# Kernel tuning notes

Hardware: AMD Instinct MI355X
Metric: run time of the kernel (lower is better)

Reference implementation:

```python
import jax, jax.numpy as jnp
import numpy as np

IN, U = 256, 512
UNFOLDS = 6

def setup_inputs() -> dict:
    key = jax.random.key(0)
    ks = jax.random.split(key, 16)
    B = 512
    inputs = jax.random.normal(ks[0], (B, IN), dtype=jnp.float32)
    state = jax.random.normal(ks[1], (B, U), dtype=jnp.float32)
    # parameters, initialized like the torch module
    sensory_mu = jax.random.uniform(ks[2], (IN, U), minval=0.3, maxval=0.8)
    sensory_sigma = jax.random.uniform(ks[3], (IN, U), minval=3.0, maxval=8.0)
    sensory_W = jax.random.uniform(ks[4], (IN, U), minval=0.01, maxval=1.0)
    sensory_erev = (2.0 * jax.random.randint(ks[5], (IN, U), 0, 2).astype(jnp.float32) - 1.0)
    mu = jax.random.uniform(ks[6], (U, U), minval=0.3, maxval=0.8)
    sigma = jax.random.uniform(ks[7], (U, U), minval=3.0, maxval=8.0)
    W = jax.random.uniform(ks[8], (U, U), minval=0.01, maxval=1.0)
    erev = (2.0 * jax.random.randint(ks[9], (U, U), 0, 2).astype(jnp.float32) - 1.0)
    vleak = jax.random.uniform(ks[10], (U,), minval=-0.2, maxval=0.2)
    gleak = jnp.ones((U,), dtype=jnp.float32)   # gleak_init_min == max == 1.0
    cm_t = jnp.full((U,), 0.5, dtype=jnp.float32)  # cm_init_min == max == 0.5
    input_w = jnp.ones((IN,), dtype=jnp.float32)
    input_b = jnp.zeros((IN,), dtype=jnp.float32)
    return dict(inputs=inputs, state=state, input_w=input_w, input_b=input_b,
                sensory_mu=sensory_mu, sensory_sigma=sensory_sigma,
                sensory_W=sensory_W, sensory_erev=sensory_erev,
                mu=mu, sigma=sigma, W=W, erev=erev,
                vleak=vleak, gleak=gleak, cm_t=cm_t)

def _syn_sigmoid(v, mu, sigma):
    # v: [B, N] -> [B, N, 1]; mu, sigma: [N, M]; result [B, N, M]
    return jax.nn.sigmoid(sigma * (v[..., None] - mu))

def reference(inputs, state, input_w, input_b, sensory_mu, sensory_sigma,
              sensory_W, sensory_erev, mu, sigma, W, erev, vleak, gleak, cm_t):
    # Affine input mapping
    x = inputs * input_w + input_b                       # [B, IN]
    # sensory synapses (computed once)
    sens_act = sensory_W * _syn_sigmoid(x, sensory_mu, sensory_sigma)  # [B, IN, U]
    w_num_s = jnp.sum(sens_act * sensory_erev, axis=1)   # [B, U]
    w_den_s = jnp.sum(sens_act, axis=1)                  # [B, U]
    # semi-implicit ODE unfold (6 fixed steps)
    v_pre = state
    for _ in range(UNFOLDS):
        w_act = W * _syn_sigmoid(v_pre, mu, sigma)       # [B, U, U]
        w_num = jnp.sum(w_act * erev, axis=1) + w_num_s  # [B, U]
        w_den = jnp.sum(w_act, axis=1) + w_den_s         # [B, U]
        numerator = cm_t * v_pre + gleak * vleak + w_num
        denominator = cm_t + gleak + w_den
        v_pre = numerator / denominator
    return v_pre  # module returns (next_state, next_state); both identical
```

## Files before the change

### kernel.cpp

```cpp
#include <hip/hip_runtime.h>

#define IN_DIM 256
#define U_DIM  512
#define L2E    1.44269504088896340736f

__global__ void k_fuse(const float* __restrict__ mu, const float* __restrict__ sigma,
                       const float* __restrict__ W, const float* __restrict__ erev,
                       const float* __restrict__ smu, const float* __restrict__ ssig,
                       const float* __restrict__ sW, const float* __restrict__ serev,
                       float2* __restrict__ sm2, float* __restrict__ wep,
                       float4* __restrict__ sf4) {
    int i = blockIdx.x * blockDim.x + threadIdx.x;
    const int UU = U_DIM * U_DIM;
    const int SU = IN_DIM * U_DIM;
    if (i < UU) {
        float s = sigma[i] * L2E;
        sm2[i] = make_float2(s, mu[i] * s);
        wep[i] = W[i] * erev[i];
    } else if (i < UU + SU) {
        int j = i - UU;
        float s = ssig[j] * L2E;
        float w = sW[j];
        sf4[j] = make_float4(s, smu[j] * s, w * serev[j], w);
    }
}

__global__ __launch_bounds__(512, 8) void k_sensory(
    const float* __restrict__ inputs, const float* __restrict__ input_w,
    const float* __restrict__ input_b, const float4* __restrict__ sf4,
    float* __restrict__ wnum_s, float* __restrict__ wden_s) {
    __shared__ __align__(16) float xs[4 * IN_DIM];
    __shared__ float red[8 * 4 * 64 * 2];
    const int tid = threadIdx.x;
    const int b0 = blockIdx.x * 4;
    const int u0 = blockIdx.y * 64;

    #pragma unroll
    for (int k = 0; k < 2; ++k) {
        int idx = tid + k * 512;
        int r = idx >> 8, i = idx & 255;
        xs[idx] = fmaf(inputs[(b0 + r) * IN_DIM + i], input_w[i], input_b[i]);
    }
    __syncthreads();

    const int ul = tid & 63;
    const int strip = tid >> 6;
    const int u = u0 + ul;
    float nacc[4], dacc[4];
    #pragma unroll
    for (int r = 0; r < 4; ++r) { nacc[r] = 0.f; dacc[r] = 0.f; }

    const int i0 = strip * 32;
    for (int ic = 0; ic < 32; ic += 4) {
        const int i = i0 + ic;
        float4 q0 = sf4[(i + 0) * U_DIM + u];
        float4 q1 = sf4[(i + 1) * U_DIM + u];
        float4 q2 = sf4[(i + 2) * U_DIM + u];
        float4 q3 = sf4[(i + 3) * U_DIM + u];
        #pragma unroll
        for (int r = 0; r < 4; ++r) {
            const float4 x4 = *reinterpret_cast<const float4*>(&xs[r * IN_DIM + i]);
            {
                float e = __builtin_amdgcn_exp2f(fmaf(-q0.x, x4.x, q0.y));
                float p = __builtin_amdgcn_rcpf(1.f + e);
                nacc[r] = fmaf(q0.z, p, nacc[r]); dacc[r] = fmaf(q0.w, p, dacc[r]);
            }
            {
                float e = __builtin_amdgcn_exp2f(fmaf(-q1.x, x4.y, q1.y));
                float p = __builtin_amdgcn_rcpf(1.f + e);
                nacc[r] = fmaf(q1.z, p, nacc[r]); dacc[r] = fmaf(q1.w, p, dacc[r]);
            }
            {
                float e = __builtin_amdgcn_exp2f(fmaf(-q2.x, x4.z, q2.y));
                float p = __builtin_amdgcn_rcpf(1.f + e);
                nacc[r] = fmaf(q2.z, p, nacc[r]); dacc[r] = fmaf(q2.w, p, dacc[r]);
            }
            {
                float e = __builtin_amdgcn_exp2f(fmaf(-q3.x, x4.w, q3.y));
                float p = __builtin_amdgcn_rcpf(1.f + e);
                nacc[r] = fmaf(q3.z, p, nacc[r]); dacc[r] = fmaf(q3.w, p, dacc[r]);
            }
        }
    }
    #pragma unroll
    for (int r = 0; r < 4; ++r) {
        red[(((strip * 4 + r) * 64) + ul) * 2 + 0] = nacc[r];
        red[(((strip * 4 + r) * 64) + ul) * 2 + 1] = dacc[r];
    }
    __syncthreads();
    if (tid < 4 * 64) {
        const int r = tid >> 6, uu = tid & 63;
        float n = 0.f, d = 0.f;
        #pragma unroll
        for (int s = 0; s < 8; ++s) {
            n += red[(((s * 4 + r) * 64) + uu) * 2 + 0];
            d += red[(((s * 4 + r) * 64) + uu) * 2 + 1];
        }
        wnum_s[(b0 + r) * U_DIM + (u0 + uu)] = n;
        wden_s[(b0 + r) * U_DIM + (u0 + uu)] = d;
    }
}

__global__ __launch_bounds__(512, 8) void k_unfold(
    const float* __restrict__ vin,
    const float2* __restrict__ sm2, const float* __restrict__ wep,
    const float* __restrict__ wnum_s, const float* __restrict__ wden_s,
    const float* __restrict__ vleak, const float* __restrict__ gleak,
    const float* __restrict__ cm, float* __restrict__ vout) {
    __shared__ __align__(16) float vs[8 * U_DIM];
    __shared__ float red_n[8 * 8 * 32];
    __shared__ float red_d[8 * 8 * 32];
    const int tid = threadIdx.x;
    const int b0 = blockIdx.x * 8;
    const int u0 = blockIdx.y * 32;

    #pragma unroll
    for (int k = 0; k < 2; ++k) {
        int idx = tid + k * 512;
        reinterpret_cast<float4*>(vs)[idx] =
            reinterpret_cast<const float4*>(vin + (size_t)b0 * U_DIM)[idx];
    }
    __syncthreads();

    const int lane = tid & 63;
    const int w = tid >> 6;
    const int ulh = lane & 31;
    const int ih = lane >> 5;
    const int strip = w * 2 + ih;
    const int u = u0 + ulh;
    const int i0 = strip * 32;

    float nacc[8], dacc[8];
    #pragma unroll
    for (int r = 0; r < 8; ++r) { nacc[r] = 0.f; dacc[r] = 0.f; }

    for (int ic = 0; ic < 32; ic += 4) {
        const int i = i0 + ic;
        float2 q0 = sm2[(i + 0) * U_DIM + u];
        float2 q1 = sm2[(i + 1) * U_DIM + u];
        float2 q2 = sm2[(i + 2) * U_DIM + u];
        float2 q3 = sm2[(i + 3) * U_DIM + u];
        float we0 = wep[(i + 0) * U_DIM + u];
        float we1 = wep[(i + 1) * U_DIM + u];
        float we2 = wep[(i + 2) * U_DIM + u];
        float we3 = wep[(i + 3) * U_DIM + u];
        float w0 = fabsf(we0), w1 = fabsf(we1), w2 = fabsf(we2), w3 = fabsf(we3);
        #pragma unroll
        for (int r = 0; r < 8; ++r) {
            const float4 v4 = *reinterpret_cast<const float4*>(&vs[r * U_DIM + i]);
            {
                float e = __builtin_amdgcn_exp2f(fmaf(-q0.x, v4.x, q0.y));
                float p = __builtin_amdgcn_rcpf(1.f + e);
                nacc[r] = fmaf(we0, p, nacc[r]); dacc[r] = fmaf(w0, p, dacc[r]);
            }
            {
                float e = __builtin_amdgcn_exp2f(fmaf(-q1.x, v4.y, q1.y));
                float p = __builtin_amdgcn_rcpf(1.f + e);
                nacc[r] = fmaf(we1, p, nacc[r]); dacc[r] = fmaf(w1, p, dacc[r]);
            }
            {
                float e = __builtin_amdgcn_exp2f(fmaf(-q2.x, v4.z, q2.y));
                float p = __builtin_amdgcn_rcpf(1.f + e);
                nacc[r] = fmaf(we2, p, nacc[r]); dacc[r] = fmaf(w2, p, dacc[r]);
            }
            {
                float e = __builtin_amdgcn_exp2f(fmaf(-q3.x, v4.w, q3.y));
                float p = __builtin_amdgcn_rcpf(1.f + e);
                nacc[r] = fmaf(we3, p, nacc[r]); dacc[r] = fmaf(w3, p, dacc[r]);
            }
        }
    }

    #pragma unroll
    for (int r = 0; r < 8; ++r) {
        nacc[r] += __shfl_xor(nacc[r], 32);
        dacc[r] += __shfl_xor(dacc[r], 32);
    }
    if (lane < 32) {
        #pragma unroll
        for (int r = 0; r < 8; ++r) {
            red_n[(w * 8 + r) * 32 + ulh] = nacc[r];
            red_d[(w * 8 + r) * 32 + ulh] = dacc[r];
        }
    }
    __syncthreads();
    if (tid < 8 * 32) {
        const int r = tid >> 5, uu = tid & 31;
        float n = 0.f, d = 0.f;
        #pragma unroll
        for (int s = 0; s < 8; ++s) {
            n += red_n[(s * 8 + r) * 32 + uu];
            d += red_d[(s * 8 + r) * 32 + uu];
        }
        const int gu = u0 + uu, gb = b0 + r;
        float vold = vs[r * U_DIM + gu];
        float gl = gleak[gu], c = cm[gu];
        float num = fmaf(c, vold, fmaf(gl, vleak[gu], n + wnum_s[gb * U_DIM + gu]));
        float den = c + gl + d + wden_s[gb * U_DIM + gu];
        vout[gb * U_DIM + gu] = num * __builtin_amdgcn_rcpf(den);
    }
}

__global__ __launch_bounds__(512) void k_mono(
    const float* __restrict__ inputs, const float* __restrict__ state,
    const float* __restrict__ input_w, const float* __restrict__ input_b,
    const float* __restrict__ smu, const float* __restrict__ ssig,
    const float* __restrict__ sW, const float* __restrict__ serev,
    const float* __restrict__ mu, const float* __restrict__ sigma,
    const float* __restrict__ W, const float* __restrict__ erev,
    const float* __restrict__ vleak, const float* __restrict__ gleak,
    const float* __restrict__ cm, float* __restrict__ out) {
    __shared__ float xs[IN_DIM];
    __shared__ float vsh[U_DIM];
    const int b = blockIdx.x, u = threadIdx.x;
    if (u < IN_DIM) xs[u] = fmaf(inputs[b * IN_DIM + u], input_w[u], input_b[u]);
    vsh[u] = state[b * U_DIM + u];
    __syncthreads();
    float ns = 0.f, ds = 0.f;
    for (int i = 0; i < IN_DIM; ++i) {
        int pi = i * U_DIM + u;
        float e = __builtin_amdgcn_exp2f((smu[pi] - xs[i]) * (ssig[pi] * L2E));
        float p = __builtin_amdgcn_rcpf(1.f + e);
        float a = sW[pi] * p;
        ns = fmaf(a, serev[pi], ns);
        ds += a;
    }
    const float c = cm[u], gl = gleak[u], glvl = gl * vleak[u];
    for (int t = 0; t < 6; ++t) {
        float n = ns, d = ds;
        for (int i = 0; i < U_DIM; ++i) {
            int pi = i * U_DIM + u;
            float e = __builtin_amdgcn_exp2f((mu[pi] - vsh[i]) * (sigma[pi] * L2E));
            float p = __builtin_amdgcn_rcpf(1.f + e);
            float a = W[pi] * p;
            n = fmaf(a, erev[pi], n);
            d += a;
        }
        float vn = (fmaf(c, vsh[u], glvl) + n) / (c + gl + d);
        __syncthreads();
        vsh[u] = vn;
        __syncthreads();
    }
    out[b * U_DIM + u] = vsh[u];
}

extern "C" void kernel_launch(void* const* d_in, const int* in_sizes, int n_in,
                              void* d_out, int out_size, void* d_ws, size_t ws_size,
                              hipStream_t stream) {
    const float* inputs  = (const float*)d_in[0];
    const float* state   = (const float*)d_in[1];
    const float* input_w = (const float*)d_in[2];
    const float* input_b = (const float*)d_in[3];
    const float* smu     = (const float*)d_in[4];
    const float* ssig    = (const float*)d_in[5];
    const float* sW      = (const float*)d_in[6];
    const float* serev   = (const float*)d_in[7];
    const float* mu      = (const float*)d_in[8];
    const float* sigma   = (const float*)d_in[9];
    const float* W       = (const float*)d_in[10];
    const float* erev    = (const float*)d_in[11];
    const float* vleak   = (const float*)d_in[12];
    const float* gleak   = (const float*)d_in[13];
    const float* cm      = (const float*)d_in[14];
    float* out = (float*)d_out;

    const int B = in_sizes[1] / U_DIM;
    const size_t BU = (size_t)B * U_DIM;
    const size_t UU = (size_t)U_DIM * U_DIM;
    const size_t SU = (size_t)IN_DIM * U_DIM;
    const size_t need = (3 * BU + 3 * UU + 4 * SU) * sizeof(float);

    if (ws_size >= need) {
        float* f      = (float*)d_ws;
        float* wnum_s = f;
        float* wden_s = f + BU;
        float* vbuf   = f + 2 * BU;
        float2* sm2   = (float2*)(f + 3 * BU);
        float* wep    = f + 3 * BU + 2 * UU;
        float4* sf4   = (float4*)(f + 3 * BU + 3 * UU);

        const int nfuse = (int)(UU + SU);
        k_fuse<<<(nfuse + 255) / 256, 256, 0, stream>>>(mu, sigma, W, erev,
                                                        smu, ssig, sW, serev,
                                                        sm2, wep, sf4);
        dim3 sgrid(B / 4, U_DIM / 64);
        k_sensory<<<sgrid, 512, 0, stream>>>(inputs, input_w, input_b, sf4, wnum_s, wden_s);
        dim3 ugrid(B / 8, U_DIM / 32);
        const float* vin = state;
        float* pong[2] = { vbuf, out };
        for (int t = 0; t < 6; ++t) {
            float* vo = pong[t & 1];
            k_unfold<<<ugrid, 512, 0, stream>>>(vin, sm2, wep, wnum_s, wden_s,
                                                vleak, gleak, cm, vo);
            vin = vo;
        }
    } else {
        k_mono<<<B, U_DIM, 0, stream>>>(inputs, state, input_w, input_b,
                                        smu, ssig, sW, serev, mu, sigma, W, erev,
                                        vleak, gleak, cm, out);
    }
}
```

Before: 210.3 us.

## Replace transcendental sigmoid with packed polynomial exp2 and shared reciprocal

```diff
diff --git a/kernel.cpp b/kernel.cpp
--- a/kernel.cpp
+++ b/kernel.cpp
@@ -3,6 +3,47 @@
 #define IN_DIM 256
 #define U_DIM  512
 #define L2E    1.44269504088896340736f
+
+typedef float f32x2 __attribute__((ext_vector_type(2)));
+typedef float f32x4 __attribute__((ext_vector_type(4)));
+
+__device__ __forceinline__ f32x2 vfma2(f32x2 a, f32x2 b, f32x2 c) {
+    return __builtin_elementwise_fma(a, b, c);
+}
+
+__device__ __forceinline__ float exp2scale(float y) {
+    unsigned s = (__float_as_uint(y) << 23) + 0x3F800000u;
+    return __uint_as_float(s);
+}
+
+__device__ __forceinline__ void quad_sig(f32x2 t01, f32x2 t23,
+                                         f32x2& p01, f32x2& p23) {
+    const float CM = 12582912.0f;
+    const float c4 = 0.00961813f, c3 = 0.05550411f,
+                c2 = 0.24022651f, c1 = 0.69314718f;
+    t01.x = fminf(fmaxf(t01.x, -100.f), 14.f);
+    t01.y = fminf(fmaxf(t01.y, -100.f), 14.f);
+    t23.x = fminf(fmaxf(t23.x, -100.f), 14.f);
+    t23.y = fminf(fmaxf(t23.y, -100.f), 14.f);
+    f32x2 y01 = t01 + (f32x2)(CM);
+    f32x2 y23 = t23 + (f32x2)(CM);
+    f32x2 f01 = t01 - (y01 - (f32x2)(CM));
+    f32x2 f23 = t23 - (y23 - (f32x2)(CM));
+    f32x2 q01 = vfma2((f32x2)(c4), f01, (f32x2)(c3));
+    f32x2 q23 = vfma2((f32x2)(c4), f23, (f32x2)(c3));
+    q01 = vfma2(q01, f01, (f32x2)(c2));  q23 = vfma2(q23, f23, (f32x2)(c2));
+    q01 = vfma2(q01, f01, (f32x2)(c1));  q23 = vfma2(q23, f23, (f32x2)(c1));
+    q01 = vfma2(q01, f01, (f32x2)(1.f)); q23 = vfma2(q23, f23, (f32x2)(1.f));
+    f32x2 sc01 = { exp2scale(y01.x), exp2scale(y01.y) };
+    f32x2 sc23 = { exp2scale(y23.x), exp2scale(y23.y) };
+    f32x2 d01 = vfma2(q01, sc01, (f32x2)(1.f));
+    f32x2 d23 = vfma2(q23, sc23, (f32x2)(1.f));
+    float a = d01.x * d01.y, b = d23.x * d23.y;
+    float R = __builtin_amdgcn_rcpf(a * b);
+    float Ra = R * a, Rb = R * b;
+    p01 = (f32x2){ Rb * d01.y, Rb * d01.x };
+    p23 = (f32x2){ Ra * d23.y, Ra * d23.x };
+}
 
 __global__ void k_fuse(const float* __restrict__ mu, const float* __restrict__ sigma,
                        const float* __restrict__ W, const float* __restrict__ erev,
@@ -25,89 +66,95 @@
     }
 }
 
-__global__ __launch_bounds__(512, 8) void k_sensory(
+__global__ __launch_bounds__(512, 4) void k_sensory(
     const float* __restrict__ inputs, const float* __restrict__ input_w,
     const float* __restrict__ input_b, const float4* __restrict__ sf4,
     float* __restrict__ wnum_s, float* __restrict__ wden_s) {
-    __shared__ __align__(16) float xs[4 * IN_DIM];
-    __shared__ float red[8 * 4 * 64 * 2];
+    __shared__ __align__(16) float xs2[IN_DIM * 8];
+    __shared__ float red_n[8 * 8 * 32];
+    __shared__ float red_d[8 * 8 * 32];
     const int tid = threadIdx.x;
-    const int b0 = blockIdx.x * 4;
-    const int u0 = blockIdx.y * 64;
+    const int b0 = blockIdx.x * 8;
+    const int u0 = blockIdx.y * 32;
 
     #pragma unroll
-    for (int k = 0; k < 2; ++k) {
+    for (int k = 0; k < 4; ++k) {
         int idx = tid + k * 512;
         int r = idx >> 8, i = idx & 255;
-        xs[idx] = fmaf(inputs[(b0 + r) * IN_DIM + i], input_w[i], input_b[i]);
-    }
-    __syncthreads();
-
-    const int ul = tid & 63;
-    const int strip = tid >> 6;
-    const int u = u0 + ul;
-    float nacc[4], dacc[4];
+        xs2[i * 8 + r] = fmaf(inputs[(b0 + r) * IN_DIM + i], input_w[i], input_b[i]);
+    }
+    __syncthreads();
+
+    const int lane = tid & 63;
+    const int w = tid >> 6;
+    const int ulh = lane & 31;
+    const int ih = lane >> 5;
+    const int strip = w * 2 + ih;
+    const int u = u0 + ulh;
+    const int i0 = strip * 16;
+
+    f32x2 na01 = {0,0}, na23 = {0,0}, na45 = {0,0}, na67 = {0,0};
+    f32x2 da01 = {0,0}, da23 = {0,0}, da45 = {0,0}, da67 = {0,0};
+
+    #pragma unroll 2
+    for (int ic = 0; ic < 16; ++ic) {
+        const int i = i0 + ic;
+        const float4 q = sf4[i * U_DIM + u];
+        const float sgn = -q.x, ms = q.y, we = q.z, wa = q.w;
+        f32x4 va = *reinterpret_cast<const f32x4*>(&xs2[i * 8]);
+        f32x4 vb = *reinterpret_cast<const f32x4*>(&xs2[i * 8 + 4]);
+        f32x2 p01, p23, p45, p67;
+        {
+            f32x2 t01 = vfma2((f32x2)(sgn), va.xy, (f32x2)(ms));
+            f32x2 t23 = vfma2((f32x2)(sgn), va.zw, (f32x2)(ms));
+            quad_sig(t01, t23, p01, p23);
+        }
+        {
+            f32x2 t45 = vfma2((f32x2)(sgn), vb.xy, (f32x2)(ms));
+            f32x2 t67 = vfma2((f32x2)(sgn), vb.zw, (f32x2)(ms));
+            quad_sig(t45, t67, p45, p67);
+        }
+        na01 = vfma2((f32x2)(we), p01, na01); da01 = vfma2((f32x2)(wa), p01, da01);
+        na23 = vfma2((f32x2)(we), p23, na23); da23 = vfma2((f32x2)(wa), p23, da23);
+        na45 = vfma2((f32x2)(we), p45, na45); da45 = vfma2((f32x2)(wa), p45, da45);
+        na67 = vfma2((f32x2)(we), p67, na67); da67 = vfma2((f32x2)(wa), p67, da67);
+    }
+
+    float nacc[8] = { na01.x, na01.y, na23.x, na23.y, na45.x, na45.y, na67.x, na67.y };
+    float dacc[8] = { da01.x, da01.y, da23.x, da23.y, da45.x, da45.y, da67.x, da67.y };
     #pragma unroll
-    for (int r = 0; r < 4; ++r) { nacc[r] = 0.f; dacc[r] = 0.f; }
-
-    const int i0 = strip * 32;
-    for (int ic = 0; ic < 32; ic += 4) {
-        const int i = i0 + ic;
-        float4 q0 = sf4[(i + 0) * U_DIM + u];
-        float4 q1 = sf4[(i + 1) * U_DIM + u];
-        float4 q2 = sf4[(i + 2) * U_DIM + u];
-        float4 q3 = sf4[(i + 3) * U_DIM + u];
+    for (int r = 0; r < 8; ++r) {
+        nacc[r] += __shfl_xor(nacc[r], 32);
+        dacc[r] += __shfl_xor(dacc[r], 32);
+    }
+    if (lane < 32) {
         #pragma unroll
-        for (int r = 0; r < 4; ++r) {
-            const float4 x4 = *reinterpret_cast<const float4*>(&xs[r * IN_DIM + i]);
-            {
-                float e = __builtin_amdgcn_exp2f(fmaf(-q0.x, x4.x, q0.y));
-                float p = __builtin_amdgcn_rcpf(1.f + e);
-                nacc[r] = fmaf(q0.z, p, nacc[r]); dacc[r] = fmaf(q0.w, p, dacc[r]);
-            }
-            {
-                float e = __builtin_amdgcn_exp2f(fmaf(-q1.x, x4.y, q1.y));
-                float p = __builtin_amdgcn_rcpf(1.f + e);
-                nacc[r] = fmaf(q1.z, p, nacc[r]); dacc[r] = fmaf(q1.w, p, dacc[r]);
-            }
-            {
-                float e = __builtin_amdgcn_exp2f(fmaf(-q2.x, x4.z, q2.y));
-                float p = __builtin_amdgcn_rcpf(1.f + e);
-                nacc[r] = fmaf(q2.z, p, nacc[r]); dacc[r] = fmaf(q2.w, p, dacc[r]);
-            }
-            {
-                float e = __builtin_amdgcn_exp2f(fmaf(-q3.x, x4.w, q3.y));
-                float p = __builtin_amdgcn_rcpf(1.f + e);
-                nacc[r] = fmaf(q3.z, p, nacc[r]); dacc[r] = fmaf(q3.w, p, dacc[r]);
-            }
-        }
-    }
-    #pragma unroll
-    for (int r = 0; r < 4; ++r) {
-        red[(((strip * 4 + r) * 64) + ul) * 2 + 0] = nacc[r];
-        red[(((strip * 4 + r) * 64) + ul) * 2 + 1] = dacc[r];
-    }
-    __syncthreads();
-    if (tid < 4 * 64) {
-        const int r = tid >> 6, uu = tid & 63;
+        for (int r = 0; r < 8; ++r) {
+            red_n[(w * 8 + r) * 32 + ulh] = nacc[r];
+            red_d[(w * 8 + r) * 32 + ulh] = dacc[r];
+        }
+    }
+    __syncthreads();
+    if (tid < 8 * 32) {
+        const int r = tid >> 5, uu = tid & 31;
         float n = 0.f, d = 0.f;
         #pragma unroll
         for (int s = 0; s < 8; ++s) {
-            n += red[(((s * 4 + r) * 64) + uu) * 2 + 0];
-            d += red[(((s * 4 + r) * 64) + uu) * 2 + 1];
+            n += red_n[(s * 8 + r) * 32 + uu];
+            d += red_d[(s * 8 + r) * 32 + uu];
         }
         wnum_s[(b0 + r) * U_DIM + (u0 + uu)] = n;
         wden_s[(b0 + r) * U_DIM + (u0 + uu)] = d;
     }
 }
 
-__global__ __launch_bounds__(512, 8) void k_unfold(
+__global__ __launch_bounds__(512, 4) void k_unfold(
     const float* __restrict__ vin,
     const float2* __restrict__ sm2, const float* __restrict__ wep,
     const float* __restrict__ wnum_s, const float* __restrict__ wden_s,
     const float* __restrict__ vleak, const float* __restrict__ gleak,
     const float* __restrict__ cm, float* __restrict__ vout) {
-    __shared__ __align__(16) float vs[8 * U_DIM];
+    __shared__ __align__(16) float vs2[U_DIM * 8];
     __shared__ float red_n[8 * 8 * 32];
     __shared__ float red_d[8 * 8 * 32];
     const int tid = threadIdx.x;
@@ -115,10 +162,10 @@
     const int u0 = blockIdx.y * 32;
 
     #pragma unroll
-    for (int k = 0; k < 2; ++k) {
+    for (int k = 0; k < 8; ++k) {
         int idx = tid + k * 512;
-        reinterpret_cast<float4*>(vs)[idx] =
-            reinterpret_cast<const float4*>(vin + (size_t)b0 * U_DIM)[idx];
+        int r = idx >> 9, i = idx & 511;
+        vs2[i * 8 + r] = vin[(size_t)b0 * U_DIM + idx];
     }
     __syncthreads();
 
@@ -130,47 +177,37 @@
     const int u = u0 + ulh;
     const int i0 = strip * 32;
 
-    float nacc[8], dacc[8];
-    #pragma unroll
-    for (int r = 0; r < 8; ++r) { nacc[r] = 0.f; dacc[r] = 0.f; }
-
-    for (int ic = 0; ic < 32; ic += 4) {
+    f32x2 na01 = {0,0}, na23 = {0,0}, na45 = {0,0}, na67 = {0,0};
+    f32x2 da01 = {0,0}, da23 = {0,0}, da45 = {0,0}, da67 = {0,0};
+
+    #pragma unroll 2
+    for (int ic = 0; ic < 32; ++ic) {
         const int i = i0 + ic;
-        float2 q0 = sm2[(i + 0) * U_DIM + u];
-        float2 q1 = sm2[(i + 1) * U_DIM + u];
-        float2 q2 = sm2[(i + 2) * U_DIM + u];
-        float2 q3 = sm2[(i + 3) * U_DIM + u];
-        float we0 = wep[(i + 0) * U_DIM + u];
-        float we1 = wep[(i + 1) * U_DIM + u];
-        float we2 = wep[(i + 2) * U_DIM + u];
-        float we3 = wep[(i + 3) * U_DIM + u];
-        float w0 = fabsf(we0), w1 = fabsf(we1), w2 = fabsf(we2), w3 = fabsf(we3);
-        #pragma unroll
-        for (int r = 0; r < 8; ++r) {
-            const float4 v4 = *reinterpret_cast<const float4*>(&vs[r * U_DIM + i]);
-            {
-                float e = __builtin_amdgcn_exp2f(fmaf(-q0.x, v4.x, q0.y));
-                float p = __builtin_amdgcn_rcpf(1.f + e);
-                nacc[r] = fmaf(we0, p, nacc[r]); dacc[r] = fmaf(w0, p, dacc[r]);
-            }
-            {
-                float e = __builtin_amdgcn_exp2f(fmaf(-q1.x, v4.y, q1.y));
-                float p = __builtin_amdgcn_rcpf(1.f + e);
-                nacc[r] = fmaf(we1, p, nacc[r]); dacc[r] = fmaf(w1, p, dacc[r]);
-            }
-            {
-                float e = __builtin_amdgcn_exp2f(fmaf(-q2.x, v4.z, q2.y));
-                float p = __builtin_amdgcn_rcpf(1.f + e);
-                nacc[r] = fmaf(we2, p, nacc[r]); dacc[r] = fmaf(w2, p, dacc[r]);
-            }
-            {
-                float e = __builtin_amdgcn_exp2f(fmaf(-q3.x, v4.w, q3.y));
-                float p = __builtin_amdgcn_rcpf(1.f + e);
-                nacc[r] = fmaf(we3, p, nacc[r]); dacc[r] = fmaf(w3, p, dacc[r]);
-            }
-        }
-    }
-
+        const float2 q = sm2[i * U_DIM + u];
+        const float we = wep[i * U_DIM + u];
+        const float wa = fabsf(we);
+        const float sgn = -q.x, ms = q.y;
+        f32x4 va = *reinterpret_cast<const f32x4*>(&vs2[i * 8]);
+        f32x4 vb = *reinterpret_cast<const f32x4*>(&vs2[i * 8 + 4]);
+        f32x2 p01, p23, p45, p67;
+        {
+            f32x2 t01 = vfma2((f32x2)(sgn), va.xy, (f32x2)(ms));
+            f32x2 t23 = vfma2((f32x2)(sgn), va.zw, (f32x2)(ms));
+            quad_sig(t01, t23, p01, p23);
+        }
+        {
+            f32x2 t45 = vfma2((f32x2)(sgn), vb.xy, (f32x2)(ms));
+            f32x2 t67 = vfma2((f32x2)(sgn), vb.zw, (f32x2)(ms));
+            quad_sig(t45, t67, p45, p67);
+        }
+        na01 = vfma2((f32x2)(we), p01, na01); da01 = vfma2((f32x2)(wa), p01, da01);
+        na23 = vfma2((f32x2)(we), p23, na23); da23 = vfma2((f32x2)(wa), p23, da23);
+        na45 = vfma2((f32x2)(we), p45, na45); da45 = vfma2((f32x2)(wa), p45, da45);
+        na67 = vfma2((f32x2)(we), p67, na67); da67 = vfma2((f32x2)(wa), p67, da67);
+    }
+
+    float nacc[8] = { na01.x, na01.y, na23.x, na23.y, na45.x, na45.y, na67.x, na67.y };
+    float dacc[8] = { da01.x, da01.y, da23.x, da23.y, da45.x, da45.y, da67.x, da67.y };
     #pragma unroll
     for (int r = 0; r < 8; ++r) {
         nacc[r] += __shfl_xor(nacc[r], 32);
@@ -193,7 +230,7 @@
             d += red_d[(s * 8 + r) * 32 + uu];
         }
         const int gu = u0 + uu, gb = b0 + r;
-        float vold = vs[r * U_DIM + gu];
+        float vold = vs2[gu * 8 + r];
         float gl = gleak[gu], c = cm[gu];
         float num = fmaf(c, vold, fmaf(gl, vleak[gu], n + wnum_s[gb * U_DIM + gu]));
         float den = c + gl + d + wden_s[gb * U_DIM + gu];
@@ -283,15 +320,14 @@
         k_fuse<<<(nfuse + 255) / 256, 256, 0, stream>>>(mu, sigma, W, erev,
                                                         smu, ssig, sW, serev,
                                                         sm2, wep, sf4);
-        dim3 sgrid(B / 4, U_DIM / 64);
-        k_sensory<<<sgrid, 512, 0, stream>>>(inputs, input_w, input_b, sf4, wnum_s, wden_s);
-        dim3 ugrid(B / 8, U_DIM / 32);
+        dim3 grid(B / 8, U_DIM / 32);
+        k_sensory<<<grid, 512, 0, stream>>>(inputs, input_w, input_b, sf4, wnum_s, wden_s);
         const float* vin = state;
         float* pong[2] = { vbuf, out };
         for (int t = 0; t < 6; ++t) {
             float* vo = pong[t & 1];
-            k_unfold<<<ugrid, 512, 0, stream>>>(vin, sm2, wep, wnum_s, wden_s,
-                                                vleak, gleak, cm, vo);
+            k_unfold<<<grid, 512, 0, stream>>>(vin, sm2, wep, wnum_s, wden_s,
+                                               vleak, gleak, cm, vo);
             vin = vo;
         }
     } else {
```

Result: slower. 306.8 us (+45.9%).
